# Kernel tuning notes

Measured on AMD Instinct MI355X. Metric: run time of the kernel, lower is better.

The kernel has to match this reference:

```python
import jax, jax.numpy as jnp
import numpy as np

N = 50000        # nodes per node type
E_ADJ = 800000   # edges per adjacency
E_DEC = 200000   # decoder edge batch
F = 128          # input feature dim
H = 64           # hidden dim (all hid_dims equal)
RT_NUM = 4       # DEDICOM relation subtypes
# relation order per stage: [(0,0),(0,1),(1,0),(1,1)]; input node type j per relation:
J_ORDER = (0, 1, 0, 1)


def setup_inputs() -> dict:
    key = jax.random.key(0)
    ks = jax.random.split(key, 16)
    inp = {
        'adj_rows': jax.random.randint(ks[0], (8, E_ADJ), 0, N, dtype=jnp.int32),
        'adj_cols': jax.random.randint(ks[1], (8, E_ADJ), 0, N, dtype=jnp.int32),
        'adj_vals': jax.random.uniform(ks[2], (8, E_ADJ), dtype=jnp.float32),
        'feat0': jax.random.normal(ks[3], (N, F), dtype=jnp.float32),
        'feat1': jax.random.normal(ks[4], (N, F), dtype=jnp.float32),
        'W1': jax.random.normal(ks[5], (4, F, H), dtype=jnp.float32) * 0.05,
        'W2': jax.random.normal(ks[6], (4, H, H), dtype=jnp.float32) * 0.05,
        'W3': jax.random.normal(ks[7], (4, H, H), dtype=jnp.float32) * 0.05,
        'W4': jax.random.normal(ks[8], (4, H, H), dtype=jnp.float32) * 0.05,
        'R_global': jax.random.normal(ks[9], (H, H), dtype=jnp.float32) * 0.05,
        'D_local': jax.random.normal(ks[10], (RT_NUM, H), dtype=jnp.float32) * 0.05,
        'edges': jax.random.randint(ks[11], (E_DEC, 2), 0, N, dtype=jnp.int32),
        'rt_k': 1,
    }
    return inp


def _gcn_stage(rows, cols, vals, x0, x1, W):
    """One multi-relation GCN layer over 4 relations [(0,0),(0,1),(1,0),(1,1)].
    rows/cols/vals: [4, E]; x0/x1: [N, Fin]; W: [4, Fin, H].
    Returns (out0, out1): per-destination-type summed, relu'd embeddings [N, H]."""
    xin = jnp.stack([x0, x1, x0, x1])                    # [4, N, Fin] per J_ORDER
    xw = jnp.einsum('knf,kfh->knh', xin, W)              # transform per relation

    def spmm(r, c, v, m):
        # sparse adj @ m : gather messages along cols, scatter-add into rows
        return jax.ops.segment_sum(m[c] * v[:, None], r, num_segments=N)

    y = jax.vmap(spmm)(rows, cols, vals, xw)             # [4, N, H]
    y = jax.nn.relu(y)                                   # activation inside each layer
    # get_embed: sum per-relation outputs grouped by destination type i
    return y[0] + y[1], y[2] + y[3]


def reference(adj_rows, adj_cols, adj_vals, feat0, feat1, W1, W2, W3, W4,
              R_global, D_local, edges, rt_k):
    r1, c1, v1 = adj_rows[:4], adj_cols[:4], adj_vals[:4]   # stage-1 adjacencies
    r2, c2, v2 = adj_rows[4:], adj_cols[4:], adj_vals[4:]   # stage-2 adjacencies

    h0, h1 = _gcn_stage(r1, c1, v1, feat0, feat1, W1)       # s1_l1
    h0, h1 = _gcn_stage(r1, c1, v1, h0, h1, W2)             # s1_l2
    h0, h1 = _gcn_stage(r2, c2, v2, h0, h1, W3)             # s2_l1
    h0, h1 = _gcn_stage(r2, c2, v2, h0, h1, W4)             # s2_l2

    # TDDecoder for rel_type = (0, 1): gather endpoints, DEDICOM bilinear score.
    er = h0[edges[:, 0]]                                    # [E, H]
    ec = h1[edges[:, 1]]                                    # [E, H]
    d = D_local[rt_k]                                       # [H]
    M = d[:, None] * R_global * d[None, :]                  # D_k R D_k
    # torch.diag(er @ M @ ec.T) == per-edge bilinear form
    preds_pos = jnp.einsum('eh,hg,eg->e', er, M, ec)        # [E]
    return preds_pos
```

## Files before the change

### kernel.cpp

```cpp
#include <hip/hip_runtime.h>

#define N_NODES 50000
#define E_ADJ   800000
#define E_DEC   200000
#define FDIM    128
#define HDIM    64
#define NP1     (N_NODES + 1)
#define NBUK    196
#define SUBS    32
#define SCAP    192
#define BCAP    (SUBS * SCAP)
#define TILE_E  1024
#define EPB     4
#define NPBLK   782

typedef _Float16 f16;
typedef __attribute__((ext_vector_type(2))) _Float16 f16x2;
typedef __attribute__((ext_vector_type(4))) _Float16 f16x4;
typedef __attribute__((ext_vector_type(8))) _Float16 f16x8;
typedef __attribute__((ext_vector_type(4))) float f32x4;

__device__ __forceinline__ int   ntl_i(const int* p)   { return __builtin_nontemporal_load(p); }
__device__ __forceinline__ float ntl_f(const float* p) { return __builtin_nontemporal_load(p); }

__global__ void part_kernel(const int* __restrict__ rows,
                            const int* __restrict__ cols,
                            const float* __restrict__ vals,
                            int* __restrict__ gcur,
                            unsigned long long* __restrict__ bucketed)
{
    const int k   = blockIdx.y;
    const int sub = blockIdx.x & (SUBS - 1);
    const int tid = threadIdx.x;
    const long long t0 = (long long)blockIdx.x * TILE_E;

    __shared__ int hist[NBUK];
    __shared__ int cur[NBUK];
    for (int i = tid; i < NBUK; i += 256) hist[i] = 0;
    __syncthreads();

    for (int it = 0; it < EPB; ++it) {
        const long long e = t0 + it * 256 + tid;
        if (e < E_ADJ) {
            const int r = rows[(size_t)k * E_ADJ + e];
            atomicAdd(&hist[r >> 8], 1);
        }
    }
    __syncthreads();

    for (int i = tid; i < NBUK; i += 256)
        cur[i] = (hist[i] > 0) ? atomicAdd(&gcur[(k * NBUK + i) * SUBS + sub], hist[i]) : 0;
    __syncthreads();

    for (int it = 0; it < EPB; ++it) {
        const long long e = t0 + it * 256 + tid;
        if (e < E_ADJ) {
            const int r = rows[(size_t)k * E_ADJ + e];
            const int b = r >> 8;
            const int pos = atomicAdd(&cur[b], 1);
            const int c = ntl_i(&cols[(size_t)k * E_ADJ + e]);
            const float v = ntl_f(&vals[(size_t)k * E_ADJ + e]);
            const unsigned meta = (unsigned)c | ((unsigned)(r & 255) << 16);
            const unsigned long long payload =
                ((unsigned long long)__float_as_uint(v) << 32) | meta;
            bucketed[(size_t)(k * NBUK + b) * BCAP + sub * SCAP + pos] = payload;
        }
    }
}

__global__ void bucket_scan(const int* __restrict__ gcur, int* __restrict__ srtbase)
{
    __shared__ int tot[4 * NBUK];
    for (int i = threadIdx.x; i < 4 * NBUK; i += 256) {
        int t = 0;
#pragma unroll
        for (int s8 = 0; s8 < SUBS; ++s8) t += gcur[i * SUBS + s8];
        tot[i] = t;
    }
    __syncthreads();
    if (threadIdx.x < 4) {
        const int k = threadIdx.x;
        int run = 0;
        for (int b = 0; b < NBUK; ++b) {
            srtbase[k * NBUK + b] = run;
            run += tot[k * NBUK + b];
        }
    }
}

__global__ void bucket_sort(const unsigned long long* __restrict__ bucketed,
                            const int* __restrict__ gcur,
                            const int* __restrict__ srtbase,
                            unsigned* __restrict__ srt,
                            int* __restrict__ row_ptr)
{
    const int b = blockIdx.x, k = blockIdx.y, tid = threadIdx.x;
    const int base = srtbase[k * NBUK + b];
    const unsigned long long* bk = bucketed + (size_t)(k * NBUK + b) * BCAP;

    __shared__ unsigned long long stage[BCAP];
    __shared__ int spref[SUBS + 1];
    __shared__ int s[256];
    __shared__ int cur[256];
    __shared__ int rcnt[256];
    rcnt[tid] = 0;
    if (tid == 0) {
        int run = 0;
        for (int s8 = 0; s8 < SUBS; ++s8) {
            spref[s8] = run;
            run += gcur[(k * NBUK + b) * SUBS + s8];
        }
        spref[SUBS] = run;
    }
    __syncthreads();
    const int cnt = spref[SUBS];

    for (int s8 = 0; s8 < SUBS; ++s8) {
        const int off = spref[s8];
        const int c8  = spref[s8 + 1] - off;
        for (int i = tid; i < c8; i += 256)
            stage[off + i] = bk[s8 * SCAP + i];
    }
    __syncthreads();

    for (int i = tid; i < cnt; i += 256)
        atomicAdd(&rcnt[((unsigned)stage[i] >> 16) & 255], 1);
    __syncthreads();

    const int v = rcnt[tid];
    s[tid] = v;
    __syncthreads();
    for (int off = 1; off < 256; off <<= 1) {
        const int t = (tid >= off) ? s[tid - off] : 0;
        __syncthreads();
        s[tid] += t;
        __syncthreads();
    }
    const int excl = s[tid] - v;

    const int n = b * 256 + tid;
    if (n < N_NODES) row_ptr[k * NP1 + n] = base + excl;
    if (b == NBUK - 1 && tid == 0) row_ptr[k * NP1 + N_NODES] = E_ADJ;
    cur[tid] = base + excl;
    __syncthreads();

    for (int i = tid; i < cnt; i += 256) {
        const unsigned long long p = stage[i];
        const unsigned meta = (unsigned)p;
        const int rl = (meta >> 16) & 255;
        const int c  = meta & 0xFFFF;
        const float val = __uint_as_float((unsigned)(p >> 32));
        union { f16 h; unsigned short us; } cv;
        cv.h = (f16)val;
        const int pos = atomicAdd(&cur[rl], 1);
        srt[(size_t)k * E_ADJ + pos] = ((unsigned)cv.us << 16) | (unsigned)c;
    }
}

__device__ __forceinline__ void gather_quads(const unsigned* __restrict__ sp,
                                             int s, int en,
                                             const f16* __restrict__ xk,
                                             int lane, float a[4])
{
    const int es = lane >> 4;
    const int hb = (lane & 15) * 4;

    for (int base = s; base < en; base += 64) {
        const int cnt = min(64, en - base);
        unsigned meta = 0;
        if (lane < cnt) meta = sp[base + lane];
        const int nq = (cnt + 3) >> 2;
        int p = 0;
        for (; p + 4 <= nq; p += 4) {
            unsigned m[4];
#pragma unroll
            for (int u = 0; u < 4; ++u)
                m[u] = __shfl(meta, (p + u) * 4 + es, 64);
            f16x4 g[4];
            float v[4];
#pragma unroll
            for (int u = 0; u < 4; ++u) {
                union { unsigned short us; f16 h; } cv;
                cv.us = (unsigned short)(m[u] >> 16);
                v[u] = (float)cv.h;
                g[u] = *(const f16x4*)(xk + (size_t)(m[u] & 0xFFFF) * HDIM + hb);
            }
#pragma unroll
            for (int u = 0; u < 4; ++u) {
                a[0] = fmaf((float)g[u][0], v[u], a[0]);
                a[1] = fmaf((float)g[u][1], v[u], a[1]);
                a[2] = fmaf((float)g[u][2], v[u], a[2]);
                a[3] = fmaf((float)g[u][3], v[u], a[3]);
            }
        }
        for (; p < nq; ++p) {
            const unsigned m = __shfl(meta, p * 4 + es, 64);
            union { unsigned short us; f16 h; } cv;
            cv.us = (unsigned short)(m >> 16);
            const float v = (float)cv.h;
            const f16x4 g = *(const f16x4*)(xk + (size_t)(m & 0xFFFF) * HDIM + hb);
            a[0] = fmaf((float)g[0], v, a[0]);
            a[1] = fmaf((float)g[1], v, a[1]);
            a[2] = fmaf((float)g[2], v, a[2]);
            a[3] = fmaf((float)g[3], v, a[3]);
        }
    }
#pragma unroll
    for (int j = 0; j < 4; ++j) {
        a[j] += __shfl_xor(a[j], 16, 64);
        a[j] += __shfl_xor(a[j], 32, 64);
    }
}

__global__ void pack_wfrag(const float* __restrict__ W, const int K,
                           f16* __restrict__ out)
{
    const int idx = blockIdx.x * 256 + threadIdx.x;
    const int j    = idx & 7;
    const int lane = (idx >> 3) & 63;
    const int kcs  = K >> 5;
    int rest = idx >> 9;
    const int kc  = rest % kcs; rest /= kcs;
    const int nt  = rest & 3;
    const int rel = rest >> 2;
    const int k   = kc * 32 + ((lane >> 4) * 8) + j;
    const int col = nt * 16 + (lane & 15);
    out[idx] = (f16)W[((size_t)rel * K + k) * HDIM + col];
}

__global__ void gemm1_mfma(const float* __restrict__ x0,
                           const float* __restrict__ x1,
                           const f16* __restrict__ wf,
                           f16* __restrict__ xw)
{
    const int wave = threadIdx.x >> 6;
    const int lane = threadIdx.x & 63;
    const int n0 = blockIdx.x * 32;
    const int q = lane >> 4, r16 = lane & 15;

    const float* xr = (wave & 1) ? x1 : x0;

    f16x8 b[4][4];
#pragma unroll
    for (int nt = 0; nt < 4; ++nt)
#pragma unroll
        for (int kc = 0; kc < 4; ++kc)
            b[nt][kc] = *(const f16x8*)(wf + (((size_t)(wave * 4 + nt) * 4 + kc) * 64 + lane) * 8);

    for (int t = 0; t < 2; ++t) {
        const int row = n0 + t * 16 + r16;
        const int rowc = row < N_NODES ? row : N_NODES - 1;
        f16x8 a[4];
#pragma unroll
        for (int kc = 0; kc < 4; ++kc) {
            const float4 lo = *(const float4*)(xr + (size_t)rowc * FDIM + kc * 32 + q * 8);
            const float4 hi = *(const float4*)(xr + (size_t)rowc * FDIM + kc * 32 + q * 8 + 4);
            f16x8 av;
            av[0] = (f16)lo.x; av[1] = (f16)lo.y; av[2] = (f16)lo.z; av[3] = (f16)lo.w;
            av[4] = (f16)hi.x; av[5] = (f16)hi.y; av[6] = (f16)hi.z; av[7] = (f16)hi.w;
            a[kc] = av;
        }
#pragma unroll
        for (int nt = 0; nt < 4; ++nt) {
            f32x4 acc = {0.f, 0.f, 0.f, 0.f};
#pragma unroll
            for (int kc = 0; kc < 4; ++kc)
                acc = __builtin_amdgcn_mfma_f32_16x16x32_f16(a[kc], b[nt][kc], acc, 0, 0, 0);
#pragma unroll
            for (int j = 0; j < 4; ++j) {
                const int n = n0 + t * 16 + q * 4 + j;
                if (n < N_NODES)
                    xw[((size_t)wave * N_NODES + n) * HDIM + nt * 16 + r16] = (f16)acc[j];
            }
        }
    }
}

__global__ void gemm2_mfma(const f16* __restrict__ agg,
                           const f16* __restrict__ wf,
                           f16* __restrict__ h0, f16* __restrict__ h1)
{
    const int wave = threadIdx.x >> 6;
    const int lane = threadIdx.x & 63;
    const int tid  = threadIdx.x;
    const int n0 = blockIdx.x * 32;
    const int q = lane >> 4, r16 = lane & 15;

    f16x8 b[4][2];
#pragma unroll
    for (int nt = 0; nt < 4; ++nt)
#pragma unroll
        for (int kc = 0; kc < 2; ++kc)
            b[nt][kc] = *(const f16x8*)(wf + (((size_t)(wave * 4 + nt) * 2 + kc) * 64 + lane) * 8);

    __shared__ f16 yt[4][16][HDIM];

    for (int t = 0; t < 2; ++t) {
        const int row = n0 + t * 16 + r16;
        const int rowc = row < N_NODES ? row : N_NODES - 1;
        f16x8 a[2];
#pragma unroll
        for (int kc = 0; kc < 2; ++kc)
            a[kc] = *(const f16x8*)(agg + ((size_t)wave * N_NODES + rowc) * HDIM + kc * 32 + q * 8);

#pragma unroll
        for (int nt = 0; nt < 4; ++nt) {
            f32x4 acc = {0.f, 0.f, 0.f, 0.f};
#pragma unroll
            for (int kc = 0; kc < 2; ++kc)
                acc = __builtin_amdgcn_mfma_f32_16x16x32_f16(a[kc], b[nt][kc], acc, 0, 0, 0);
#pragma unroll
            for (int j = 0; j < 4; ++j)
                yt[wave][q * 4 + j][nt * 16 + r16] = (f16)fmaxf(acc[j], 0.f);
        }
        __syncthreads();

        {
            const int r  = tid >> 4;
            const int c4 = (tid & 15) * 4;
            const int n  = n0 + t * 16 + r;
            if (n < N_NODES) {
                const f16x4 a0 = *(const f16x4*)&yt[0][r][c4];
                const f16x4 a1 = *(const f16x4*)&yt[1][r][c4];
                const f16x4 a2 = *(const f16x4*)&yt[2][r][c4];
                const f16x4 a3 = *(const f16x4*)&yt[3][r][c4];
                f16x4 o0, o1;
#pragma unroll
                for (int u = 0; u < 4; ++u) {
                    o0[u] = (f16)((float)a0[u] + (float)a1[u]);
                    o1[u] = (f16)((float)a2[u] + (float)a3[u]);
                }
                *(f16x4*)(h0 + (size_t)n * HDIM + c4) = o0;
                *(f16x4*)(h1 + (size_t)n * HDIM + c4) = o1;
            }
        }
        __syncthreads();
    }
}

__global__ void spmm_csr(const unsigned* __restrict__ srt,
                         const int*    __restrict__ row_ptr,
                         const f16*    __restrict__ xw,
                         f16* __restrict__ y)
{
    const int b = blockIdx.x, k = b & 3, g = b >> 2;
    const int wave = threadIdx.x >> 6, lane = threadIdx.x & 63;
    const int n = g * 4 + wave;

    const int s  = row_ptr[k * NP1 + n];
    const int en = row_ptr[k * NP1 + n + 1];
    float a[4] = {0.f, 0.f, 0.f, 0.f};
    gather_quads(srt + (size_t)k * E_ADJ, s, en,
                 xw + (size_t)k * N_NODES * HDIM, lane, a);
    if (lane < 16) {
        f16x4 o;
        o[0] = (f16)fmaxf(a[0], 0.f);
        o[1] = (f16)fmaxf(a[1], 0.f);
        o[2] = (f16)fmaxf(a[2], 0.f);
        o[3] = (f16)fmaxf(a[3], 0.f);
        *(f16x4*)(y + ((size_t)k * N_NODES + n) * HDIM + lane * 4) = o;
    }
}

__global__ void combine_kernel(const f16* __restrict__ y,
                               f16* __restrict__ h0, f16* __restrict__ h1)
{
    const size_t NHh = (size_t)N_NODES * HDIM / 2;
    const size_t i = (size_t)blockIdx.x * 256 + threadIdx.x;
    const f16x2 a = ((const f16x2*)y)[i];
    const f16x2 b = ((const f16x2*)y)[NHh + i];
    const f16x2 c = ((const f16x2*)y)[2 * NHh + i];
    const f16x2 d = ((const f16x2*)y)[3 * NHh + i];
    f16x2 o0, o1;
    o0.x = (f16)((float)a.x + (float)b.x);
    o0.y = (f16)((float)a.y + (float)b.y);
    o1.x = (f16)((float)c.x + (float)d.x);
    o1.y = (f16)((float)c.y + (float)d.y);
    ((f16x2*)h0)[i] = o0;
    ((f16x2*)h1)[i] = o1;
}

__global__ void agg_csr(const unsigned* __restrict__ srt,
                        const int*    __restrict__ row_ptr,
                        const f16*    __restrict__ h0,
                        const f16*    __restrict__ h1,
                        f16* __restrict__ agg)
{
    const int b = blockIdx.x, k = b & 3, g = b >> 2;
    const int wave = threadIdx.x >> 6, lane = threadIdx.x & 63;
    const int n = g * 4 + wave;

    const int s  = row_ptr[k * NP1 + n];
    const int en = row_ptr[k * NP1 + n + 1];
    const f16* xk = (k & 1) ? h1 : h0;
    float a[4] = {0.f, 0.f, 0.f, 0.f};
    gather_quads(srt + (size_t)k * E_ADJ, s, en, xk, lane, a);
    if (lane < 16) {
        f16x4 o;
        o[0] = (f16)a[0];
        o[1] = (f16)a[1];
        o[2] = (f16)a[2];
        o[3] = (f16)a[3];
        *(f16x4*)(agg + ((size_t)k * N_NODES + n) * HDIM + lane * 4) = o;
    }
}

__global__ void make_M(const float* __restrict__ R, const float* __restrict__ Dl,
                       const int* __restrict__ rt_k, float* __restrict__ M)
{
    const int i = blockIdx.x * blockDim.x + threadIdx.x;
    if (i >= HDIM * HDIM) return;
    const float* d = Dl + rt_k[0] * HDIM;
    M[i] = d[i >> 6] * R[i] * d[i & 63];
}

__global__ void h0M_kernel(const f16* __restrict__ h0, const float* __restrict__ M,
                           f16* __restrict__ A)
{
    const int wave = threadIdx.x >> 6, lane = threadIdx.x & 63;
    const int n0 = blockIdx.x * 16;

    __shared__ float sx[16][HDIM];
    for (int i = threadIdx.x; i < 16 * HDIM; i += 256)
        sx[i >> 6][i & 63] = (float)h0[(size_t)n0 * HDIM + i];
    __syncthreads();

    float acc[4] = {0.f, 0.f, 0.f, 0.f};
#pragma unroll 4
    for (int f = 0; f < HDIM; ++f) {
        const float w = M[f * HDIM + lane];
#pragma unroll
        for (int r = 0; r < 4; ++r)
            acc[r] = fmaf(sx[wave * 4 + r][f], w, acc[r]);
    }
#pragma unroll
    for (int r = 0; r < 4; ++r)
        A[(size_t)(n0 + wave * 4 + r) * HDIM + lane] = (f16)acc[r];
}

__global__ void decode(const f16* __restrict__ A, const f16* __restrict__ h1,
                       const int* __restrict__ edges, float* __restrict__ out)
{
    const int w = (blockIdx.x * 256 + threadIdx.x) >> 6;
    const int lane = threadIdx.x & 63;
    const int e = w * 4 + (lane >> 4);
    const int q = lane & 15;

    const int i = edges[2 * (size_t)e];
    const int j = edges[2 * (size_t)e + 1];

    const f16x4 a = *(const f16x4*)(A + (size_t)i * HDIM + q * 4);
    const f16x4 b = *(const f16x4*)(h1 + (size_t)j * HDIM + q * 4);
    float p = 0.f;
#pragma unroll
    for (int u = 0; u < 4; ++u)
        p = fmaf((float)a[u], (float)b[u], p);
    p += __shfl_xor(p, 1, 64);
    p += __shfl_xor(p, 2, 64);
    p += __shfl_xor(p, 4, 64);
    p += __shfl_xor(p, 8, 64);
    if (q == 0) out[e] = p;
}

static void build_csr(const int* rows, const int* cols, const float* vals,
                      int* gcur, int* srtbase, unsigned long long* bucketed,
                      unsigned* srt, int* row_ptr, hipStream_t stream)
{
    hipMemsetAsync(gcur, 0, 4 * NBUK * SUBS * sizeof(int), stream);
    part_kernel<<<dim3(NPBLK, 4), 256, 0, stream>>>(rows, cols, vals, gcur, bucketed);
    bucket_scan<<<1, 256, 0, stream>>>(gcur, srtbase);
    bucket_sort<<<dim3(NBUK, 4), 256, 0, stream>>>(bucketed, gcur, srtbase, srt, row_ptr);
}

extern "C" void kernel_launch(void* const* d_in, const int* in_sizes, int n_in,
                              void* d_out, int out_size, void* d_ws, size_t ws_size,
                              hipStream_t stream) {
    const int*   adj_rows = (const int*)  d_in[0];
    const int*   adj_cols = (const int*)  d_in[1];
    const float* adj_vals = (const float*)d_in[2];
    const float* feat0    = (const float*)d_in[3];
    const float* feat1    = (const float*)d_in[4];
    const float* W1       = (const float*)d_in[5];
    const float* W2       = (const float*)d_in[6];
    const float* W3       = (const float*)d_in[7];
    const float* W4       = (const float*)d_in[8];
    const float* Rg       = (const float*)d_in[9];
    const float* Dl       = (const float*)d_in[10];
    const int*   edges    = (const int*)  d_in[11];
    const int*   rt_k     = (const int*)  d_in[12];
    float* out = (float*)d_out;

    const size_t NH = (size_t)N_NODES * HDIM;
    float* ws = (float*)d_ws;
    f16*      xwh     = (f16*)ws;
    f16*      h0      = (f16*)(ws + 2 * NH);
    f16*      h1      = (f16*)(ws + 2 * NH + NH / 2);
    unsigned* srt     = (unsigned*)(ws + 3 * NH);
    int*      row_ptr = (int*)(ws + 3 * NH + 8 * (size_t)E_ADJ);
    int*      gcur    = row_ptr + 4 * NP1 + 60;
    int*      srtbase = gcur + 4 * NBUK * SUBS;
    float*    M       = (float*)(srtbase + 4 * NBUK + 32);
    unsigned long long* bucketed =
        (unsigned long long*)(M + HDIM * HDIM + 64);
    f16* y = (f16*)bucketed;
    f16* wfrag = (f16*)(bucketed + (size_t)4 * NBUK * BCAP);
    f16* wf1 = wfrag;
    f16* wf2 = wfrag + 32768;
    f16* wf3 = wfrag + 49152;
    f16* wf4 = wfrag + 65536;

    const int* r2 = adj_rows + 4 * (size_t)E_ADJ;
    const int* c2 = adj_cols + 4 * (size_t)E_ADJ;
    const float* v2 = adj_vals + 4 * (size_t)E_ADJ;

    pack_wfrag<<<128, 256, 0, stream>>>(W1, FDIM, wf1);
    pack_wfrag<<<64, 256, 0, stream>>>(W2, HDIM, wf2);
    pack_wfrag<<<64, 256, 0, stream>>>(W3, HDIM, wf3);
    pack_wfrag<<<64, 256, 0, stream>>>(W4, HDIM, wf4);

    build_csr(adj_rows, adj_cols, adj_vals, gcur, srtbase, bucketed, srt, row_ptr, stream);

    gemm1_mfma<<<1563, 256, 0, stream>>>(feat0, feat1, wf1, xwh);
    spmm_csr<<<N_NODES, 256, 0, stream>>>(srt, row_ptr, xwh, y);
    combine_kernel<<<(int)(NH / 2 / 256), 256, 0, stream>>>(y, h0, h1);

    agg_csr<<<N_NODES, 256, 0, stream>>>(srt, row_ptr, h0, h1, xwh);
    gemm2_mfma<<<1563, 256, 0, stream>>>(xwh, wf2, h0, h1);

    build_csr(r2, c2, v2, gcur, srtbase, bucketed, srt, row_ptr, stream);

    agg_csr<<<N_NODES, 256, 0, stream>>>(srt, row_ptr, h0, h1, xwh);
    gemm2_mfma<<<1563, 256, 0, stream>>>(xwh, wf3, h0, h1);

    agg_csr<<<N_NODES, 256, 0, stream>>>(srt, row_ptr, h0, h1, xwh);
    gemm2_mfma<<<1563, 256, 0, stream>>>(xwh, wf4, h0, h1);

    make_M<<<(HDIM * HDIM + 255) / 256, 256, 0, stream>>>(Rg, Dl, rt_k, M);
    f16* A = xwh;
    h0M_kernel<<<N_NODES / 16, 256, 0, stream>>>(h0, M, A);
    decode<<<E_DEC * 16 / 256, 256, 0, stream>>>(A, h1, edges, out);
}
```

Measured before the change: 566.1 us.

## Gather rows with 16-byte loads, 8 edges per wave step; drop LDS staging in bucket sort

The SpMM gather now has each lane load 8 halves (16 bytes) from a row, so one wave step covers 8 edges instead of 4 with wider vector loads, and the reduction gains an extra shuffle stage. The bucket-sort kernel no longer stages bucket entries in a large shared-memory array and instead reads them from global memory twice, which lowers LDS use and may raise occupancy at the cost of a second global read. The new gather loop processes octets in pairs without a remainder guard, so an odd octet count reads a row chosen by a lane whose meta is 0. That extra read is wasted work.

```diff
diff --git a/kernel.cpp b/kernel.cpp
--- a/kernel.cpp
+++ b/kernel.cpp
@@ -98,33 +98,21 @@
     const int base = srtbase[k * NBUK + b];
     const unsigned long long* bk = bucketed + (size_t)(k * NBUK + b) * BCAP;
 
-    __shared__ unsigned long long stage[BCAP];
-    __shared__ int spref[SUBS + 1];
+    __shared__ int scnt[SUBS];
     __shared__ int s[256];
     __shared__ int cur[256];
     __shared__ int rcnt[256];
     rcnt[tid] = 0;
-    if (tid == 0) {
-        int run = 0;
-        for (int s8 = 0; s8 < SUBS; ++s8) {
-            spref[s8] = run;
-            run += gcur[(k * NBUK + b) * SUBS + s8];
-        }
-        spref[SUBS] = run;
-    }
-    __syncthreads();
-    const int cnt = spref[SUBS];
+    if (tid < SUBS) scnt[tid] = gcur[(k * NBUK + b) * SUBS + tid];
+    __syncthreads();
 
     for (int s8 = 0; s8 < SUBS; ++s8) {
-        const int off = spref[s8];
-        const int c8  = spref[s8 + 1] - off;
-        for (int i = tid; i < c8; i += 256)
-            stage[off + i] = bk[s8 * SCAP + i];
-    }
-    __syncthreads();
-
-    for (int i = tid; i < cnt; i += 256)
-        atomicAdd(&rcnt[((unsigned)stage[i] >> 16) & 255], 1);
+        const int c8 = scnt[s8];
+        for (int i = tid; i < c8; i += 256) {
+            const unsigned meta = (unsigned)bk[s8 * SCAP + i];
+            atomicAdd(&rcnt[(meta >> 16) & 255], 1);
+        }
+    }
     __syncthreads();
 
     const int v = rcnt[tid];
@@ -144,69 +132,56 @@
     cur[tid] = base + excl;
     __syncthreads();
 
-    for (int i = tid; i < cnt; i += 256) {
-        const unsigned long long p = stage[i];
-        const unsigned meta = (unsigned)p;
-        const int rl = (meta >> 16) & 255;
-        const int c  = meta & 0xFFFF;
-        const float val = __uint_as_float((unsigned)(p >> 32));
-        union { f16 h; unsigned short us; } cv;
-        cv.h = (f16)val;
-        const int pos = atomicAdd(&cur[rl], 1);
-        srt[(size_t)k * E_ADJ + pos] = ((unsigned)cv.us << 16) | (unsigned)c;
-    }
-}
-
-__device__ __forceinline__ void gather_quads(const unsigned* __restrict__ sp,
-                                             int s, int en,
-                                             const f16* __restrict__ xk,
-                                             int lane, float a[4])
-{
-    const int es = lane >> 4;
-    const int hb = (lane & 15) * 4;
+    for (int s8 = 0; s8 < SUBS; ++s8) {
+        const int c8 = scnt[s8];
+        for (int i = tid; i < c8; i += 256) {
+            const unsigned long long p = bk[s8 * SCAP + i];
+            const unsigned meta = (unsigned)p;
+            const int rl = (meta >> 16) & 255;
+            const int c  = meta & 0xFFFF;
+            const float val = __uint_as_float((unsigned)(p >> 32));
+            union { f16 h; unsigned short us; } cv;
+            cv.h = (f16)val;
+            const int pos = atomicAdd(&cur[rl], 1);
+            srt[(size_t)k * E_ADJ + pos] = ((unsigned)cv.us << 16) | (unsigned)c;
+        }
+    }
+}
+
+__device__ __forceinline__ void gather_octs(const unsigned* __restrict__ sp,
+                                            int s, int en,
+                                            const f16* __restrict__ xk,
+                                            int lane, float a[8])
+{
+    const int es = lane >> 3;
+    const int hb = (lane & 7) * 8;
 
     for (int base = s; base < en; base += 64) {
         const int cnt = min(64, en - base);
         unsigned meta = 0;
         if (lane < cnt) meta = sp[base + lane];
-        const int nq = (cnt + 3) >> 2;
-        int p = 0;
-        for (; p + 4 <= nq; p += 4) {
-            unsigned m[4];
-#pragma unroll
-            for (int u = 0; u < 4; ++u)
-                m[u] = __shfl(meta, (p + u) * 4 + es, 64);
-            f16x4 g[4];
-            float v[4];
-#pragma unroll
-            for (int u = 0; u < 4; ++u) {
-                union { unsigned short us; f16 h; } cv;
-                cv.us = (unsigned short)(m[u] >> 16);
-                v[u] = (float)cv.h;
-                g[u] = *(const f16x4*)(xk + (size_t)(m[u] & 0xFFFF) * HDIM + hb);
-            }
-#pragma unroll
-            for (int u = 0; u < 4; ++u) {
-                a[0] = fmaf((float)g[u][0], v[u], a[0]);
-                a[1] = fmaf((float)g[u][1], v[u], a[1]);
-                a[2] = fmaf((float)g[u][2], v[u], a[2]);
-                a[3] = fmaf((float)g[u][3], v[u], a[3]);
-            }
-        }
-        for (; p < nq; ++p) {
-            const unsigned m = __shfl(meta, p * 4 + es, 64);
-            union { unsigned short us; f16 h; } cv;
-            cv.us = (unsigned short)(m >> 16);
-            const float v = (float)cv.h;
-            const f16x4 g = *(const f16x4*)(xk + (size_t)(m & 0xFFFF) * HDIM + hb);
-            a[0] = fmaf((float)g[0], v, a[0]);
-            a[1] = fmaf((float)g[1], v, a[1]);
-            a[2] = fmaf((float)g[2], v, a[2]);
-            a[3] = fmaf((float)g[3], v, a[3]);
-        }
-    }
-#pragma unroll
-    for (int j = 0; j < 4; ++j) {
+        const int no = (cnt + 7) >> 3;
+        for (int p = 0; p < no; p += 2) {
+            const unsigned m0 = __shfl(meta, p * 8 + es, 64);
+            const unsigned m1 = __shfl(meta, (p + 1) * 8 + es, 64);
+            union { unsigned short us; f16 h; } c0, c1;
+            c0.us = (unsigned short)(m0 >> 16);
+            c1.us = (unsigned short)(m1 >> 16);
+            const float v0 = (float)c0.h;
+            const float v1 = (float)c1.h;
+            const f16x8 g0 = *(const f16x8*)(xk + (size_t)(m0 & 0xFFFF) * HDIM + hb);
+            const f16x8 g1 = *(const f16x8*)(xk + (size_t)(m1 & 0xFFFF) * HDIM + hb);
+#pragma unroll
+            for (int j = 0; j < 8; ++j)
+                a[j] = fmaf((float)g0[j], v0, a[j]);
+#pragma unroll
+            for (int j = 0; j < 8; ++j)
+                a[j] = fmaf((float)g1[j], v1, a[j]);
+        }
+    }
+#pragma unroll
+    for (int j = 0; j < 8; ++j) {
+        a[j] += __shfl_xor(a[j], 8, 64);
         a[j] += __shfl_xor(a[j], 16, 64);
         a[j] += __shfl_xor(a[j], 32, 64);
     }
@@ -349,16 +324,15 @@
 
     const int s  = row_ptr[k * NP1 + n];
     const int en = row_ptr[k * NP1 + n + 1];
-    float a[4] = {0.f, 0.f, 0.f, 0.f};
-    gather_quads(srt + (size_t)k * E_ADJ, s, en,
-                 xw + (size_t)k * N_NODES * HDIM, lane, a);
-    if (lane < 16) {
-        f16x4 o;
-        o[0] = (f16)fmaxf(a[0], 0.f);
-        o[1] = (f16)fmaxf(a[1], 0.f);
-        o[2] = (f16)fmaxf(a[2], 0.f);
-        o[3] = (f16)fmaxf(a[3], 0.f);
-        *(f16x4*)(y + ((size_t)k * N_NODES + n) * HDIM + lane * 4) = o;
+    float a[8] = {0.f, 0.f, 0.f, 0.f, 0.f, 0.f, 0.f, 0.f};
+    gather_octs(srt + (size_t)k * E_ADJ, s, en,
+                xw + (size_t)k * N_NODES * HDIM, lane, a);
+    if (lane < 8) {
+        f16x8 o;
+#pragma unroll
+        for (int j = 0; j < 8; ++j)
+            o[j] = (f16)fmaxf(a[j], 0.f);
+        *(f16x8*)(y + ((size_t)k * N_NODES + n) * HDIM + lane * 8) = o;
     }
 }
 
@@ -393,15 +367,14 @@
     const int s  = row_ptr[k * NP1 + n];
     const int en = row_ptr[k * NP1 + n + 1];
     const f16* xk = (k & 1) ? h1 : h0;
-    float a[4] = {0.f, 0.f, 0.f, 0.f};
-    gather_quads(srt + (size_t)k * E_ADJ, s, en, xk, lane, a);
-    if (lane < 16) {
-        f16x4 o;
-        o[0] = (f16)a[0];
-        o[1] = (f16)a[1];
-        o[2] = (f16)a[2];
-        o[3] = (f16)a[3];
-        *(f16x4*)(agg + ((size_t)k * N_NODES + n) * HDIM + lane * 4) = o;
+    float a[8] = {0.f, 0.f, 0.f, 0.f, 0.f, 0.f, 0.f, 0.f};
+    gather_octs(srt + (size_t)k * E_ADJ, s, en, xk, lane, a);
+    if (lane < 8) {
+        f16x8 o;
+#pragma unroll
+        for (int j = 0; j < 8; ++j)
+            o[j] = (f16)a[j];
+        *(f16x8*)(agg + ((size_t)k * N_NODES + n) * HDIM + lane * 8) = o;
     }
 }
 
```

After: 560.4 us. About the same (-1.0%).
